# Kernel tuning notes

Measured on AMD Instinct MI355X. Metric: run time of the kernel, lower is better.

## Reference

```python
import jax, jax.numpy as jnp
import numpy as np

N_NODES = 50000
N_EDGES = 800000
IN_DIM = 128
HID = 128
N_LAYERS = 2


def setup_inputs() -> dict:
    key = jax.random.key(0)
    ks = jax.random.split(key, 16)
    x = jax.random.normal(ks[0], (N_NODES, IN_DIM), dtype=jnp.float32)
    edge_index = jax.random.randint(ks[1], (2, N_EDGES), 0, N_NODES, dtype=jnp.int64)
    def lin(k, fan_in, fan_out):
        bound = 1.0 / np.sqrt(fan_in)
        k1, k2 = jax.random.split(k)
        W = jax.random.uniform(k1, (fan_in, fan_out), jnp.float32, -bound, bound)
        b = jax.random.uniform(k2, (fan_out,), jnp.float32, -bound, bound)
        return W, b
    W1_0, b1_0 = lin(ks[2], IN_DIM, HID)
    W2_0, b2_0 = lin(ks[3], HID, HID)
    W1_1, b1_1 = lin(ks[4], HID, HID)
    W2_1, b2_1 = lin(ks[5], HID, HID)
    Wr, br = lin(ks[6], HID, 1)
    return dict(x=x, edge_index=edge_index,
                W1_0=W1_0, b1_0=b1_0, W2_0=W2_0, b2_0=b2_0,
                W1_1=W1_1, b1_1=b1_1, W2_1=W2_1, b2_1=b2_1,
                Wr=Wr, br=br)


def _gin_conv(x, src, dst, W1, b1, W2, b2):
    # GINConv (eps=0): h = MLP(x + sum_{j in N(i)} x_j)
    msgs = x[src]                                   # [E, d] gather
    agg = jax.ops.segment_sum(msgs, dst, num_segments=x.shape[0])  # [N, d] scatter-add
    h = x + agg
    h = jax.nn.relu(h @ W1 + b1)
    return h @ W2 + b2


def reference(x, edge_index, W1_0, b1_0, W2_0, b2_0, W1_1, b1_1, W2_1, b2_1, Wr, br):
    src, dst = edge_index[0], edge_index[1]
    # layer 0
    h = jax.nn.relu(_gin_conv(x, src, dst, W1_0, b1_0, W2_0, b2_0))
    # layer 1 (dropout is identity in eval mode)
    h = jax.nn.relu(_gin_conv(h, src, dst, W1_1, b1_1, W2_1, b2_1))
    return h @ Wr + br
```

## Files before the change

### kernel.cpp

```cpp
#include <hip/hip_runtime.h>

#define HIDDEN 128
#define NB_SHIFT 7
#define NPB 128
#define EPB 4096

typedef __attribute__((ext_vector_type(8))) short short8;
typedef __attribute__((ext_vector_type(4))) float f32x4;
typedef _Float16 f16;
typedef __attribute__((ext_vector_type(8))) _Float16 f16x8;

__device__ __forceinline__ ushort f2bf(float a) {
  union { float f; unsigned u; } c; c.f = a;
  return (ushort)((c.u + 0x7FFFu + ((c.u >> 16) & 1u)) >> 16);
}
__device__ __forceinline__ float bf2f(ushort h) {
  union { unsigned u; float f; } c; c.u = ((unsigned)h) << 16;
  return c.f;
}

__global__ __launch_bounds__(256) void bucket_hist_kernel(
    const int* __restrict__ dst, int* __restrict__ bcnt, int E, int NB) {
  __shared__ int loc[512];
  const int t = threadIdx.x;
  loc[t] = 0; loc[t + 256] = 0;
  __syncthreads();
  const int base = blockIdx.x * EPB;
  const int end = min(base + EPB, E);
  for (int e = base + t; e < end; e += 256)
    atomicAdd(&loc[dst[e] >> NB_SHIFT], 1);
  __syncthreads();
  for (int b = t; b < NB; b += 256)
    if (loc[b]) atomicAdd(&bcnt[b], loc[b]);
}

__global__ __launch_bounds__(256) void scan_buckets_kernel(
    const int* __restrict__ bcnt, int* __restrict__ pairOff,
    int* __restrict__ gCursor, int NB) {
  __shared__ int sh[512];
  const int t = threadIdx.x;
  const int v0 = (t < NB) ? bcnt[t] : 0;
  const int v1 = (t + 256 < NB) ? bcnt[t + 256] : 0;
  sh[t] = v0; sh[t + 256] = v1;
  __syncthreads();
#pragma unroll
  for (int off = 1; off < 512; off <<= 1) {
    int a = (t >= off) ? sh[t - off] : 0;
    int b = (t + 256 >= off) ? sh[t + 256 - off] : 0;
    __syncthreads();
    sh[t] += a; sh[t + 256] += b;
    __syncthreads();
  }
  const int e0 = sh[t] - v0;
  const int e1 = sh[t + 256] - v1;
  pairOff[t] = e0; gCursor[t] = e0;
  pairOff[t + 256] = e1; gCursor[t + 256] = e1;
  if (t == 255) pairOff[512] = sh[511];
}

__global__ __launch_bounds__(256) void partition_kernel(
    const int* __restrict__ src, const int* __restrict__ dst,
    int* __restrict__ gCursor, int* __restrict__ pairs, int E, int NB) {
  __shared__ int loc[512];
  __shared__ int cur[512];
  const int t = threadIdx.x;
  loc[t] = 0; loc[t + 256] = 0;
  __syncthreads();
  const int base = blockIdx.x * EPB;
  const int end = min(base + EPB, E);
  for (int e = base + t; e < end; e += 256)
    atomicAdd(&loc[dst[e] >> NB_SHIFT], 1);
  __syncthreads();
  for (int b = t; b < NB; b += 256)
    cur[b] = loc[b] ? atomicAdd(&gCursor[b], loc[b]) : 0;
  __syncthreads();
  for (int e = base + t; e < end; e += 256) {
    const int d = dst[e];
    const int p = atomicAdd(&cur[d >> NB_SHIFT], 1);
    pairs[p] = ((d & (NPB - 1)) << 25) | src[e];
  }
}

__global__ __launch_bounds__(256) void build_csr_kernel(
    const int* __restrict__ pairs, const int* __restrict__ pairOff,
    int* __restrict__ rowptr, int* __restrict__ col, int M, int E, int NB) {
  __shared__ int deg[NPB];
  __shared__ int pre[NPB];
  __shared__ int cur[NPB];
  const int b = blockIdx.x;
  const int t = threadIdx.x;
  const int s = pairOff[b];
  const int e2 = pairOff[b + 1];
  const int nodeBase = b << NB_SHIFT;
  const int nNodes = min(NPB, M - nodeBase);
  if (t < NPB) deg[t] = 0;
  __syncthreads();
  for (int i = s + t; i < e2; i += 256)
    atomicAdd(&deg[((unsigned)pairs[i]) >> 25], 1);
  __syncthreads();
  if (t < NPB) pre[t] = deg[t];
  __syncthreads();
#pragma unroll
  for (int off = 1; off < NPB; off <<= 1) {
    int v = (t < NPB && t >= off) ? pre[t - off] : 0;
    __syncthreads();
    if (t < NPB) pre[t] += v;
    __syncthreads();
  }
  if (t < nNodes) rowptr[nodeBase + t] = s + pre[t] - deg[t];
  if (b == NB - 1 && t == 0) rowptr[M] = E;
  if (t < NPB) cur[t] = pre[t] - deg[t];
  __syncthreads();
  for (int i = s + t; i < e2; i += 256) {
    const int pr = pairs[i];
    const int pos = s + atomicAdd(&cur[((unsigned)pr) >> 25], 1);
    col[pos] = pr & 0x1FFFFFF;
  }
}

__global__ __launch_bounds__(256) void f2h_kernel(const float* __restrict__ in,
                                                  f16* __restrict__ out, int n8) {
  int i = blockIdx.x * 256 + threadIdx.x;
  if (i >= n8) return;
  const float4* p = (const float4*)(in + (size_t)i * 8);
  float4 a = p[0], b = p[1];
  f16x8 o;
  o[0] = (f16)a.x; o[1] = (f16)a.y; o[2] = (f16)a.z; o[3] = (f16)a.w;
  o[4] = (f16)b.x; o[5] = (f16)b.y; o[6] = (f16)b.z; o[7] = (f16)b.w;
  *(f16x8*)(out + (size_t)i * 8) = o;
}

__global__ __launch_bounds__(256) void prepack_kernel(
    const float* __restrict__ Wa, const float* __restrict__ Wb,
    const float* __restrict__ Wc, const float* __restrict__ Wd,
    ushort* __restrict__ out) {
  int idx = blockIdx.x * 256 + threadIdx.x;
  int w = idx >> 11;
  int rem = idx & 2047;
  int ks = rem >> 9;
  int nf = (rem >> 6) & 7;
  int lane = rem & 63;
  const float* W = (w == 0) ? Wa : (w == 1) ? Wb : (w == 2) ? Wc : Wd;
  const int kbase = ks * 32 + (lane >> 4) * 8;
  const int n = nf * 16 + (lane & 15);
  ushort* oh = out + (size_t)w * 32768 + (size_t)rem * 8;
  ushort* ol = oh + 16384;
#pragma unroll
  for (int j = 0; j < 8; ++j) {
    float v = W[(size_t)(kbase + j) * HIDDEN + n];
    ushort h = f2bf(v);
    oh[j] = h;
    ol[j] = f2bf(v - bf2f(h));
  }
}

__global__ __launch_bounds__(128, 4) void gin_layer_kernel(
    const f16* __restrict__ xh, const int* __restrict__ rowptr,
    const int* __restrict__ col, const ushort* __restrict__ W1p,
    const float* __restrict__ b1, const ushort* __restrict__ W2p,
    const float* __restrict__ b2, f16* __restrict__ Ch,
    const float* __restrict__ Wr, const float* __restrict__ br,
    float* __restrict__ outv, int M, int doReadout) {
  __shared__ float buf[16][132];
  __shared__ float pr[16];
  const int t = threadIdx.x;
  const int lane = t & 63;
  const int h = t >> 6;
  const int r = lane & 15;
  const int g = lane >> 4;
  const int mBase = blockIdx.x * 16;
  int arow = mBase + r;
  if (arow > M - 1) arow = M - 1;

  float a32[4][8];
  if (h == 0) {
    const f16* rp = xh + (size_t)arow * HIDDEN + g * 8;
    f16x8 s0 = *(const f16x8*)(rp);
    f16x8 s1 = *(const f16x8*)(rp + 32);
    f16x8 s2 = *(const f16x8*)(rp + 64);
    f16x8 s3 = *(const f16x8*)(rp + 96);
#pragma unroll
    for (int j = 0; j < 8; ++j) {
      a32[0][j] = (float)s0[j]; a32[1][j] = (float)s1[j];
      a32[2][j] = (float)s2[j]; a32[3][j] = (float)s3[j];
    }
  } else {
#pragma unroll
    for (int ks = 0; ks < 4; ++ks)
#pragma unroll
      for (int j = 0; j < 8; ++j) a32[ks][j] = 0.f;
  }
  {
    const int sAll = rowptr[arow];
    const int eAll = rowptr[arow + 1];
    const int mid = sAll + ((eAll - sAll) >> 1);
    const int s = h ? mid : sAll;
    const int e = h ? eAll : mid;
    int i = s;
    for (; i + 1 < e; i += 2) {
      const int c0 = col[i], c1 = col[i + 1];
      const f16* p0 = xh + (size_t)c0 * HIDDEN + g * 8;
      const f16* p1 = xh + (size_t)c1 * HIDDEN + g * 8;
      f16x8 u0 = *(const f16x8*)(p0);
      f16x8 u1 = *(const f16x8*)(p0 + 32);
      f16x8 u2 = *(const f16x8*)(p0 + 64);
      f16x8 u3 = *(const f16x8*)(p0 + 96);
      f16x8 v0 = *(const f16x8*)(p1);
      f16x8 v1 = *(const f16x8*)(p1 + 32);
      f16x8 v2 = *(const f16x8*)(p1 + 64);
      f16x8 v3 = *(const f16x8*)(p1 + 96);
#pragma unroll
      for (int j = 0; j < 8; ++j) {
        a32[0][j] += (float)u0[j] + (float)v0[j];
        a32[1][j] += (float)u1[j] + (float)v1[j];
        a32[2][j] += (float)u2[j] + (float)v2[j];
        a32[3][j] += (float)u3[j] + (float)v3[j];
      }
    }
    if (i < e) {
      const int c0 = col[i];
      const f16* p0 = xh + (size_t)c0 * HIDDEN + g * 8;
      f16x8 u0 = *(const f16x8*)(p0);
      f16x8 u1 = *(const f16x8*)(p0 + 32);
      f16x8 u2 = *(const f16x8*)(p0 + 64);
      f16x8 u3 = *(const f16x8*)(p0 + 96);
#pragma unroll
      for (int j = 0; j < 8; ++j) {
        a32[0][j] += (float)u0[j];
        a32[1][j] += (float)u1[j];
        a32[2][j] += (float)u2[j];
        a32[3][j] += (float)u3[j];
      }
    }
  }

  if (h == 1) {
#pragma unroll
    for (int ks = 0; ks < 4; ++ks) {
      *(float4*)&buf[r][ks * 32 + g * 8] =
          make_float4(a32[ks][0], a32[ks][1], a32[ks][2], a32[ks][3]);
      *(float4*)&buf[r][ks * 32 + g * 8 + 4] =
          make_float4(a32[ks][4], a32[ks][5], a32[ks][6], a32[ks][7]);
    }
  }
  __syncthreads();
  if (h == 0) {
#pragma unroll
    for (int ks = 0; ks < 4; ++ks) {
      float4 q0 = *(const float4*)&buf[r][ks * 32 + g * 8];
      float4 q1 = *(const float4*)&buf[r][ks * 32 + g * 8 + 4];
      a32[ks][0] += q0.x; a32[ks][1] += q0.y; a32[ks][2] += q0.z; a32[ks][3] += q0.w;
      a32[ks][4] += q1.x; a32[ks][5] += q1.y; a32[ks][6] += q1.z; a32[ks][7] += q1.w;
    }
  }
  __syncthreads();
  if (h == 0) {
#pragma unroll
    for (int ks = 0; ks < 4; ++ks) {
      *(float4*)&buf[r][ks * 32 + g * 8] =
          make_float4(a32[ks][0], a32[ks][1], a32[ks][2], a32[ks][3]);
      *(float4*)&buf[r][ks * 32 + g * 8 + 4] =
          make_float4(a32[ks][4], a32[ks][5], a32[ks][6], a32[ks][7]);
    }
  }
  __syncthreads();
  if (h == 1) {
#pragma unroll
    for (int ks = 0; ks < 4; ++ks) {
      float4 q0 = *(const float4*)&buf[r][ks * 32 + g * 8];
      float4 q1 = *(const float4*)&buf[r][ks * 32 + g * 8 + 4];
      a32[ks][0] = q0.x; a32[ks][1] = q0.y; a32[ks][2] = q0.z; a32[ks][3] = q0.w;
      a32[ks][4] = q1.x; a32[ks][5] = q1.y; a32[ks][6] = q1.z; a32[ks][7] = q1.w;
    }
  }
  __syncthreads();

  f32x4 acc[4];
#pragma unroll
  for (int i = 0; i < 4; ++i) acc[i] = (f32x4){0.f, 0.f, 0.f, 0.f};

#pragma unroll
  for (int ks = 0; ks < 4; ++ks) {
    short8 ah, al;
#pragma unroll
    for (int j = 0; j < 8; ++j) {
      ushort hh = f2bf(a32[ks][j]);
      ah[j] = (short)hh;
      al[j] = (short)f2bf(a32[ks][j] - bf2f(hh));
    }
#pragma unroll
    for (int nfi = 0; nfi < 4; ++nfi) {
      const ushort* bp = W1p + ((size_t)(ks * 8 + h * 4 + nfi) * 64 + lane) * 8;
      short8 bh = *(const short8*)bp;
      short8 bl = *(const short8*)(bp + 16384);
      acc[nfi] = __builtin_amdgcn_mfma_f32_16x16x32_bf16(ah, bh, acc[nfi], 0, 0, 0);
      acc[nfi] = __builtin_amdgcn_mfma_f32_16x16x32_bf16(al, bh, acc[nfi], 0, 0, 0);
      acc[nfi] = __builtin_amdgcn_mfma_f32_16x16x32_bf16(ah, bl, acc[nfi], 0, 0, 0);
    }
  }

#pragma unroll
  for (int nfi = 0; nfi < 4; ++nfi) {
    const int nf = h * 4 + nfi;
    float bv = b1[nf * 16 + r];
#pragma unroll
    for (int q = 0; q < 4; ++q)
      buf[g * 4 + q][nf * 16 + r] = fmaxf(acc[nfi][q] + bv, 0.f);
    acc[nfi] = (f32x4){0.f, 0.f, 0.f, 0.f};
  }
  __syncthreads();

#pragma unroll
  for (int ks = 0; ks < 4; ++ks) {
    const float* hp = &buf[r][ks * 32 + g * 8];
    float4 a0 = *(const float4*)hp;
    float4 a1 = *(const float4*)(hp + 4);
    float av[8] = {a0.x, a0.y, a0.z, a0.w, a1.x, a1.y, a1.z, a1.w};
    short8 ah, al;
#pragma unroll
    for (int j = 0; j < 8; ++j) {
      ushort hh = f2bf(av[j]);
      ah[j] = (short)hh;
      al[j] = (short)f2bf(av[j] - bf2f(hh));
    }
#pragma unroll
    for (int nfi = 0; nfi < 4; ++nfi) {
      const ushort* bp = W2p + ((size_t)(ks * 8 + h * 4 + nfi) * 64 + lane) * 8;
      short8 bh = *(const short8*)bp;
      short8 bl = *(const short8*)(bp + 16384);
      acc[nfi] = __builtin_amdgcn_mfma_f32_16x16x32_bf16(ah, bh, acc[nfi], 0, 0, 0);
      acc[nfi] = __builtin_amdgcn_mfma_f32_16x16x32_bf16(al, bh, acc[nfi], 0, 0, 0);
      acc[nfi] = __builtin_amdgcn_mfma_f32_16x16x32_bf16(ah, bl, acc[nfi], 0, 0, 0);
    }
  }

  if (!doReadout) {
    __syncthreads();
#pragma unroll
    for (int nfi = 0; nfi < 4; ++nfi) {
      const int nf = h * 4 + nfi;
      float bv = b2[nf * 16 + r];
#pragma unroll
      for (int q = 0; q < 4; ++q)
        buf[g * 4 + q][nf * 16 + r] = fmaxf(acc[nfi][q] + bv, 0.f);
    }
    __syncthreads();
    const int rr = t >> 3;
    const int gm = mBase + rr;
    if (gm < M) {
#pragma unroll
      for (int i = 0; i < 2; ++i) {
        const int c0 = (t & 7) * 8 + i * 64;
        float4 v0 = *(const float4*)&buf[rr][c0];
        float4 v1 = *(const float4*)&buf[rr][c0 + 4];
        f16x8 o;
        o[0] = (f16)v0.x; o[1] = (f16)v0.y; o[2] = (f16)v0.z; o[3] = (f16)v0.w;
        o[4] = (f16)v1.x; o[5] = (f16)v1.y; o[6] = (f16)v1.z; o[7] = (f16)v1.w;
        *(f16x8*)(Ch + (size_t)gm * HIDDEN + c0) = o;
      }
    }
  } else {
    float p[4] = {0.f, 0.f, 0.f, 0.f};
#pragma unroll
    for (int nfi = 0; nfi < 4; ++nfi) {
      const int nf = h * 4 + nfi;
      float bv = b2[nf * 16 + r];
      float wv = Wr[nf * 16 + r];
#pragma unroll
      for (int q = 0; q < 4; ++q) {
        float hv = fmaxf(acc[nfi][q] + bv, 0.f);
        p[q] += hv * wv;
      }
    }
#pragma unroll
    for (int q = 0; q < 4; ++q) {
      p[q] += __shfl_xor(p[q], 8);
      p[q] += __shfl_xor(p[q], 4);
      p[q] += __shfl_xor(p[q], 2);
      p[q] += __shfl_xor(p[q], 1);
    }
    if (h == 1 && r == 0) {
#pragma unroll
      for (int q = 0; q < 4; ++q) pr[g * 4 + q] = p[q];
    }
    __syncthreads();
    if (h == 0 && r == 0) {
      float brv = br[0];
#pragma unroll
      for (int q = 0; q < 4; ++q) {
        int gm = mBase + g * 4 + q;
        if (gm < M) outv[gm] = p[q] + pr[g * 4 + q] + brv;
      }
    }
  }
}

extern "C" void kernel_launch(void* const* d_in, const int* in_sizes, int n_in,
                              void* d_out, int out_size, void* d_ws,
                              size_t ws_size, hipStream_t stream) {
  const float* x = (const float*)d_in[0];
  const int* ei = (const int*)d_in[1];
  const float* W1_0 = (const float*)d_in[2];
  const float* b1_0 = (const float*)d_in[3];
  const float* W2_0 = (const float*)d_in[4];
  const float* b2_0 = (const float*)d_in[5];
  const float* W1_1 = (const float*)d_in[6];
  const float* b1_1 = (const float*)d_in[7];
  const float* W2_1 = (const float*)d_in[8];
  const float* b2_1 = (const float*)d_in[9];
  const float* Wr = (const float*)d_in[10];
  const float* br = (const float*)d_in[11];

  const int M = in_sizes[0] / HIDDEN;
  const int E = in_sizes[1] / 2;
  const int* src = ei;
  const int* dst = ei + E;
  const int NB = (M + NPB - 1) >> NB_SHIFT;

  int* pairs = (int*)d_ws;
  f16* xh = (f16*)(pairs + E);
  f16* Bh = xh + (size_t)M * HIDDEN;
  int* rowptr = (int*)(Bh + (size_t)M * HIDDEN);
  int* col = rowptr + M + 1;
  int* bcnt = col + E;
  int* pairOff = bcnt + 512;
  int* gCursor = pairOff + 513;
  ushort* Wpk = (ushort*)(gCursor + 512);

  const int ginBlocks = (M + 15) / 16;
  const int cvtBlocks = (M * 16 + 255) / 256;
  const int edgeBlocks = (E + EPB - 1) / EPB;
  float* out = (float*)d_out;

  prepack_kernel<<<32, 256, 0, stream>>>(W1_0, W2_0, W1_1, W2_1, Wpk);
  f2h_kernel<<<cvtBlocks, 256, 0, stream>>>(x, xh, M * 16);

  hipMemsetAsync(bcnt, 0, 512 * sizeof(int), stream);
  bucket_hist_kernel<<<edgeBlocks, 256, 0, stream>>>(dst, bcnt, E, NB);
  scan_buckets_kernel<<<1, 256, 0, stream>>>(bcnt, pairOff, gCursor, NB);
  partition_kernel<<<edgeBlocks, 256, 0, stream>>>(src, dst, gCursor, pairs,
                                                   E, NB);
  build_csr_kernel<<<NB, 256, 0, stream>>>(pairs, pairOff, rowptr, col, M, E,
                                           NB);

  gin_layer_kernel<<<ginBlocks, 128, 0, stream>>>(
      xh, rowptr, col, Wpk, b1_0, Wpk + 32768, b2_0, Bh,
      nullptr, nullptr, nullptr, M, 0);

  gin_layer_kernel<<<ginBlocks, 128, 0, stream>>>(
      Bh, rowptr, col, Wpk + 65536, b1_1, Wpk + 98304, b2_1, nullptr,
      Wr, br, out, M, 1);
}
```

Baseline: 234.0 us.

## Split GIN layer work across four waves per 16-row block

Each 16-node block now uses four wavefronts instead of two. The neighbor gather is split into quarters, partial sums are combined through a tree reduction in two shared buffers, and each wave computes two of the eight output column tiles of both MLP matmuls. The aim is more memory-level parallelism on the irregular gather and less matmul work per wave. In exchange it adds extra LDS traffic and barriers, and every wave redundantly converts the full A operand to split bf16.

```diff
diff --git a/kernel.cpp b/kernel.cpp
--- a/kernel.cpp
+++ b/kernel.cpp
@@ -154,18 +154,19 @@
   }
 }
 
-__global__ __launch_bounds__(128, 4) void gin_layer_kernel(
+__global__ __launch_bounds__(256, 4) void gin_layer_kernel(
     const f16* __restrict__ xh, const int* __restrict__ rowptr,
     const int* __restrict__ col, const ushort* __restrict__ W1p,
     const float* __restrict__ b1, const ushort* __restrict__ W2p,
     const float* __restrict__ b2, f16* __restrict__ Ch,
     const float* __restrict__ Wr, const float* __restrict__ br,
     float* __restrict__ outv, int M, int doReadout) {
-  __shared__ float buf[16][132];
-  __shared__ float pr[16];
+  __shared__ float bufA[16][132];
+  __shared__ float bufB[16][132];
+  __shared__ float pr[3][16];
   const int t = threadIdx.x;
   const int lane = t & 63;
-  const int h = t >> 6;
+  const int w = t >> 6;
   const int r = lane & 15;
   const int g = lane >> 4;
   const int mBase = blockIdx.x * 16;
@@ -173,7 +174,7 @@
   if (arow > M - 1) arow = M - 1;
 
   float a32[4][8];
-  if (h == 0) {
+  if (w == 0) {
     const f16* rp = xh + (size_t)arow * HIDDEN + g * 8;
     f16x8 s0 = *(const f16x8*)(rp);
     f16x8 s1 = *(const f16x8*)(rp + 32);
@@ -192,10 +193,9 @@
   }
   {
     const int sAll = rowptr[arow];
-    const int eAll = rowptr[arow + 1];
-    const int mid = sAll + ((eAll - sAll) >> 1);
-    const int s = h ? mid : sAll;
-    const int e = h ? eAll : mid;
+    const int len = rowptr[arow + 1] - sAll;
+    const int s = sAll + ((len * w) >> 2);
+    const int e = sAll + ((len * (w + 1)) >> 2);
     int i = s;
     for (; i + 1 < e; i += 2) {
       const int c0 = col[i], c1 = col[i + 1];
@@ -234,50 +234,65 @@
     }
   }
 
-  if (h == 1) {
+  if (w == 1 || w == 3) {
+    float (*dstb)[132] = (w == 1) ? bufA : bufB;
 #pragma unroll
     for (int ks = 0; ks < 4; ++ks) {
-      *(float4*)&buf[r][ks * 32 + g * 8] =
+      *(float4*)&dstb[r][ks * 32 + g * 8] =
           make_float4(a32[ks][0], a32[ks][1], a32[ks][2], a32[ks][3]);
-      *(float4*)&buf[r][ks * 32 + g * 8 + 4] =
+      *(float4*)&dstb[r][ks * 32 + g * 8 + 4] =
           make_float4(a32[ks][4], a32[ks][5], a32[ks][6], a32[ks][7]);
     }
   }
   __syncthreads();
-  if (h == 0) {
+  if (w == 0 || w == 2) {
+    float (*srcb)[132] = (w == 0) ? bufA : bufB;
 #pragma unroll
     for (int ks = 0; ks < 4; ++ks) {
-      float4 q0 = *(const float4*)&buf[r][ks * 32 + g * 8];
-      float4 q1 = *(const float4*)&buf[r][ks * 32 + g * 8 + 4];
+      float4 q0 = *(const float4*)&srcb[r][ks * 32 + g * 8];
+      float4 q1 = *(const float4*)&srcb[r][ks * 32 + g * 8 + 4];
       a32[ks][0] += q0.x; a32[ks][1] += q0.y; a32[ks][2] += q0.z; a32[ks][3] += q0.w;
       a32[ks][4] += q1.x; a32[ks][5] += q1.y; a32[ks][6] += q1.z; a32[ks][7] += q1.w;
     }
   }
   __syncthreads();
-  if (h == 0) {
+  if (w == 2) {
 #pragma unroll
     for (int ks = 0; ks < 4; ++ks) {
-      *(float4*)&buf[r][ks * 32 + g * 8] =
+      *(float4*)&bufA[r][ks * 32 + g * 8] =
           make_float4(a32[ks][0], a32[ks][1], a32[ks][2], a32[ks][3]);
-      *(float4*)&buf[r][ks * 32 + g * 8 + 4] =
+      *(float4*)&bufA[r][ks * 32 + g * 8 + 4] =
           make_float4(a32[ks][4], a32[ks][5], a32[ks][6], a32[ks][7]);
     }
   }
   __syncthreads();
-  if (h == 1) {
+  if (w == 0) {
 #pragma unroll
     for (int ks = 0; ks < 4; ++ks) {
-      float4 q0 = *(const float4*)&buf[r][ks * 32 + g * 8];
-      float4 q1 = *(const float4*)&buf[r][ks * 32 + g * 8 + 4];
+      float4 q0 = *(const float4*)&bufA[r][ks * 32 + g * 8];
+      float4 q1 = *(const float4*)&bufA[r][ks * 32 + g * 8 + 4];
+      a32[ks][0] += q0.x; a32[ks][1] += q0.y; a32[ks][2] += q0.z; a32[ks][3] += q0.w;
+      a32[ks][4] += q1.x; a32[ks][5] += q1.y; a32[ks][6] += q1.z; a32[ks][7] += q1.w;
+      *(float4*)&bufB[r][ks * 32 + g * 8] =
+          make_float4(a32[ks][0], a32[ks][1], a32[ks][2], a32[ks][3]);
+      *(float4*)&bufB[r][ks * 32 + g * 8 + 4] =
+          make_float4(a32[ks][4], a32[ks][5], a32[ks][6], a32[ks][7]);
+    }
+  }
+  __syncthreads();
+  if (w != 0) {
+#pragma unroll
+    for (int ks = 0; ks < 4; ++ks) {
+      float4 q0 = *(const float4*)&bufB[r][ks * 32 + g * 8];
+      float4 q1 = *(const float4*)&bufB[r][ks * 32 + g * 8 + 4];
       a32[ks][0] = q0.x; a32[ks][1] = q0.y; a32[ks][2] = q0.z; a32[ks][3] = q0.w;
       a32[ks][4] = q1.x; a32[ks][5] = q1.y; a32[ks][6] = q1.z; a32[ks][7] = q1.w;
     }
   }
-  __syncthreads();
-
-  f32x4 acc[4];
-#pragma unroll
-  for (int i = 0; i < 4; ++i) acc[i] = (f32x4){0.f, 0.f, 0.f, 0.f};
+
+  f32x4 acc[2];
+#pragma unroll
+  for (int i = 0; i < 2; ++i) acc[i] = (f32x4){0.f, 0.f, 0.f, 0.f};
 
 #pragma unroll
   for (int ks = 0; ks < 4; ++ks) {
@@ -289,8 +304,8 @@
       al[j] = (short)f2bf(a32[ks][j] - bf2f(hh));
     }
 #pragma unroll
-    for (int nfi = 0; nfi < 4; ++nfi) {
-      const ushort* bp = W1p + ((size_t)(ks * 8 + h * 4 + nfi) * 64 + lane) * 8;
+    for (int nfi = 0; nfi < 2; ++nfi) {
+      const ushort* bp = W1p + ((size_t)(ks * 8 + w * 2 + nfi) * 64 + lane) * 8;
       short8 bh = *(const short8*)bp;
       short8 bl = *(const short8*)(bp + 16384);
       acc[nfi] = __builtin_amdgcn_mfma_f32_16x16x32_bf16(ah, bh, acc[nfi], 0, 0, 0);
@@ -298,21 +313,22 @@
       acc[nfi] = __builtin_amdgcn_mfma_f32_16x16x32_bf16(ah, bl, acc[nfi], 0, 0, 0);
     }
   }
-
-#pragma unroll
-  for (int nfi = 0; nfi < 4; ++nfi) {
-    const int nf = h * 4 + nfi;
+  __syncthreads();
+
+#pragma unroll
+  for (int nfi = 0; nfi < 2; ++nfi) {
+    const int nf = w * 2 + nfi;
     float bv = b1[nf * 16 + r];
 #pragma unroll
     for (int q = 0; q < 4; ++q)
-      buf[g * 4 + q][nf * 16 + r] = fmaxf(acc[nfi][q] + bv, 0.f);
+      bufA[g * 4 + q][nf * 16 + r] = fmaxf(acc[nfi][q] + bv, 0.f);
     acc[nfi] = (f32x4){0.f, 0.f, 0.f, 0.f};
   }
   __syncthreads();
 
 #pragma unroll
   for (int ks = 0; ks < 4; ++ks) {
-    const float* hp = &buf[r][ks * 32 + g * 8];
+    const float* hp = &bufA[r][ks * 32 + g * 8];
     float4 a0 = *(const float4*)hp;
     float4 a1 = *(const float4*)(hp + 4);
     float av[8] = {a0.x, a0.y, a0.z, a0.w, a1.x, a1.y, a1.z, a1.w};
@@ -324,8 +340,8 @@
       al[j] = (short)f2bf(av[j] - bf2f(hh));
     }
 #pragma unroll
-    for (int nfi = 0; nfi < 4; ++nfi) {
-      const ushort* bp = W2p + ((size_t)(ks * 8 + h * 4 + nfi) * 64 + lane) * 8;
+    for (int nfi = 0; nfi < 2; ++nfi) {
+      const ushort* bp = W2p + ((size_t)(ks * 8 + w * 2 + nfi) * 64 + lane) * 8;
       short8 bh = *(const short8*)bp;
       short8 bl = *(const short8*)(bp + 16384);
       acc[nfi] = __builtin_amdgcn_mfma_f32_16x16x32_bf16(ah, bh, acc[nfi], 0, 0, 0);
@@ -335,35 +351,31 @@
   }
 
   if (!doReadout) {
-    __syncthreads();
-#pragma unroll
-    for (int nfi = 0; nfi < 4; ++nfi) {
-      const int nf = h * 4 + nfi;
+#pragma unroll
+    for (int nfi = 0; nfi < 2; ++nfi) {
+      const int nf = w * 2 + nfi;
       float bv = b2[nf * 16 + r];
 #pragma unroll
       for (int q = 0; q < 4; ++q)
-        buf[g * 4 + q][nf * 16 + r] = fmaxf(acc[nfi][q] + bv, 0.f);
-    }
-    __syncthreads();
-    const int rr = t >> 3;
+        bufB[g * 4 + q][nf * 16 + r] = fmaxf(acc[nfi][q] + bv, 0.f);
+    }
+    __syncthreads();
+    const int rr = t >> 4;
+    const int c0 = (t & 15) * 8;
     const int gm = mBase + rr;
     if (gm < M) {
-#pragma unroll
-      for (int i = 0; i < 2; ++i) {
-        const int c0 = (t & 7) * 8 + i * 64;
-        float4 v0 = *(const float4*)&buf[rr][c0];
-        float4 v1 = *(const float4*)&buf[rr][c0 + 4];
-        f16x8 o;
-        o[0] = (f16)v0.x; o[1] = (f16)v0.y; o[2] = (f16)v0.z; o[3] = (f16)v0.w;
-        o[4] = (f16)v1.x; o[5] = (f16)v1.y; o[6] = (f16)v1.z; o[7] = (f16)v1.w;
-        *(f16x8*)(Ch + (size_t)gm * HIDDEN + c0) = o;
-      }
+      float4 v0 = *(const float4*)&bufB[rr][c0];
+      float4 v1 = *(const float4*)&bufB[rr][c0 + 4];
+      f16x8 o;
+      o[0] = (f16)v0.x; o[1] = (f16)v0.y; o[2] = (f16)v0.z; o[3] = (f16)v0.w;
+      o[4] = (f16)v1.x; o[5] = (f16)v1.y; o[6] = (f16)v1.z; o[7] = (f16)v1.w;
+      *(f16x8*)(Ch + (size_t)gm * HIDDEN + c0) = o;
     }
   } else {
     float p[4] = {0.f, 0.f, 0.f, 0.f};
 #pragma unroll
-    for (int nfi = 0; nfi < 4; ++nfi) {
-      const int nf = h * 4 + nfi;
+    for (int nfi = 0; nfi < 2; ++nfi) {
+      const int nf = w * 2 + nfi;
       float bv = b2[nf * 16 + r];
       float wv = Wr[nf * 16 + r];
 #pragma unroll
@@ -379,17 +391,19 @@
       p[q] += __shfl_xor(p[q], 2);
       p[q] += __shfl_xor(p[q], 1);
     }
-    if (h == 1 && r == 0) {
-#pragma unroll
-      for (int q = 0; q < 4; ++q) pr[g * 4 + q] = p[q];
-    }
-    __syncthreads();
-    if (h == 0 && r == 0) {
+    if (w != 0 && r == 0) {
+#pragma unroll
+      for (int q = 0; q < 4; ++q) pr[w - 1][g * 4 + q] = p[q];
+    }
+    __syncthreads();
+    if (w == 0 && r == 0) {
       float brv = br[0];
 #pragma unroll
       for (int q = 0; q < 4; ++q) {
         int gm = mBase + g * 4 + q;
-        if (gm < M) outv[gm] = p[q] + pr[g * 4 + q] + brv;
+        if (gm < M)
+          outv[gm] = p[q] + pr[0][g * 4 + q] + pr[1][g * 4 + q] +
+                     pr[2][g * 4 + q] + brv;
       }
     }
   }
@@ -443,11 +457,11 @@
   build_csr_kernel<<<NB, 256, 0, stream>>>(pairs, pairOff, rowptr, col, M, E,
                                            NB);
 
-  gin_layer_kernel<<<ginBlocks, 128, 0, stream>>>(
+  gin_layer_kernel<<<ginBlocks, 256, 0, stream>>>(
       xh, rowptr, col, Wpk, b1_0, Wpk + 32768, b2_0, Bh,
       nullptr, nullptr, nullptr, M, 0);
 
-  gin_layer_kernel<<<ginBlocks, 128, 0, stream>>>(
+  gin_layer_kernel<<<ginBlocks, 256, 0, stream>>>(
       Bh, rowptr, col, Wpk + 65536, b1_1, Wpk + 98304, b2_1, nullptr,
       Wr, br, out, M, 1);
 }
```

After: 241.8 us. +3.3%, slower.
